# Kernel tuning notes

Measured on AMD Instinct MI355X. Metric: run time of the kernel, lower is better.

The kernel has to match this reference:

```python
import jax, jax.numpy as jnp
import numpy as np

N_NODES = 100000
N_EDGES = 1_000_000
NODE_DIM = 64
EDGE_DIM = 32
HIDDEN = 64


def _unif(key, shape, fan_in):
    bound = 1.0 / np.sqrt(fan_in)
    return jax.random.uniform(key, shape, jnp.float32, -bound, bound)


def setup_inputs() -> dict:
    key = jax.random.key(0)
    ks = jax.random.split(key, 11)
    node_features = jax.random.normal(ks[0], (N_NODES, NODE_DIM), jnp.float32)
    edge_index = jax.random.randint(ks[1], (2, N_EDGES), 0, N_NODES, dtype=jnp.int64)
    edge_features = jax.random.normal(ks[2], (N_EDGES, EDGE_DIM), jnp.float32)
    in_dim = 2 * NODE_DIM + EDGE_DIM
    # message MLP: Linear(in_dim, HIDDEN) -> ReLU -> Linear(HIDDEN, HIDDEN)
    W1 = _unif(ks[3], (HIDDEN, in_dim), in_dim)
    b1 = _unif(ks[4], (HIDDEN,), in_dim)
    W2 = _unif(ks[5], (HIDDEN, HIDDEN), HIDDEN)
    b2 = _unif(ks[6], (HIDDEN,), HIDDEN)
    # GRUCell(input=HIDDEN, hidden=NODE_DIM); gates stacked [r; z; n]
    w_ih = _unif(ks[7], (3 * NODE_DIM, HIDDEN), NODE_DIM)
    w_hh = _unif(ks[8], (3 * NODE_DIM, NODE_DIM), NODE_DIM)
    b_ih = _unif(ks[9], (3 * NODE_DIM,), NODE_DIM)
    b_hh = _unif(ks[10], (3 * NODE_DIM,), NODE_DIM)
    return {
        "node_features": node_features,
        "edge_index": edge_index,
        "edge_features": edge_features,
        "W1": W1, "b1": b1, "W2": W2, "b2": b2,
        "w_ih": w_ih, "w_hh": w_hh, "b_ih": b_ih, "b_hh": b_hh,
    }


def reference(node_features, edge_index, edge_features, W1, b1, W2, b2, w_ih, w_hh, b_ih, b_hh):
    src, dst = edge_index[0], edge_index[1]
    # gather endpoints and build message MLP input: [E, 2*node_dim+edge_dim]
    x = jnp.concatenate([node_features[src], node_features[dst], edge_features], axis=-1)
    h = jax.nn.relu(x @ W1.T + b1)
    messages = h @ W2.T + b2  # [E, HIDDEN]
    # scatter-add into per-node aggregates
    agg = jax.ops.segment_sum(messages, dst, num_segments=node_features.shape[0])
    # GRUCell(agg, node_features) with torch gate order [r, z, n]
    gi = agg @ w_ih.T + b_ih
    gh = node_features @ w_hh.T + b_hh
    i_r, i_z, i_n = jnp.split(gi, 3, axis=-1)
    h_r, h_z, h_n = jnp.split(gh, 3, axis=-1)
    r = jax.nn.sigmoid(i_r + h_r)
    z = jax.nn.sigmoid(i_z + h_z)
    n = jnp.tanh(i_n + r * h_n)
    return (1.0 - z) * n + z * node_features
```

## Files before the change

kernel.cpp:

```cpp
#include <hip/hip_runtime.h>
#include <hip/hip_bf16.h>

#define N_NODES 100000
#define N_EDGES 1000000

typedef __bf16 bf16x8 __attribute__((ext_vector_type(8)));
typedef float  f32x4  __attribute__((ext_vector_type(4)));

#define MFMA(a, b, c) __builtin_amdgcn_mfma_f32_16x16x32_bf16((a), (b), (c), 0, 0, 0)

__device__ __forceinline__ float sigmoid_f(float x) { return 1.f / (1.f + __expf(-x)); }
__device__ __forceinline__ float tanh_f(float x) {
    float cx = fminf(fmaxf(x, -30.f), 30.f);
    float e = __expf(-2.f * cx);
    return (1.f - e) / (1.f + e);
}

__global__ __launch_bounds__(256) void pq_kernel(
    const float* __restrict__ nf, const float* __restrict__ W1,
    const float* __restrict__ b1,
    __bf16* __restrict__ Pb, __bf16* __restrict__ Qb)
{
    const int lane = threadIdx.x & 63;
    const int r = lane & 15, g = lane >> 4;

    bf16x8 Bs[4][2], Bd[4][2];
    #pragma unroll
    for (int nt = 0; nt < 4; ++nt)
        #pragma unroll
        for (int kk = 0; kk < 2; ++kk) {
            const float* ws = &W1[(nt * 16 + r) * 160 + kk * 32 + g * 8];
            const float* wd = ws + 64;
            f32x4 s0 = *(const f32x4*)ws, s1 = *(const f32x4*)(ws + 4);
            f32x4 d0 = *(const f32x4*)wd, d1 = *(const f32x4*)(wd + 4);
            #pragma unroll
            for (int j = 0; j < 4; ++j) {
                Bs[nt][kk][j] = (__bf16)s0[j]; Bs[nt][kk][j + 4] = (__bf16)s1[j];
                Bd[nt][kk][j] = (__bf16)d0[j]; Bd[nt][kk][j + 4] = (__bf16)d1[j];
            }
        }
    float b1v[4];
    #pragma unroll
    for (int nt = 0; nt < 4; ++nt) b1v[nt] = b1[nt * 16 + r];

    const int wid = blockIdx.x * (blockDim.x >> 6) + (threadIdx.x >> 6);
    const int nW  = gridDim.x * (blockDim.x >> 6);
    for (int t = wid; t < N_NODES / 16; t += nW) {
        const int base = t * 16;
        bf16x8 A[2];
        #pragma unroll
        for (int kk = 0; kk < 2; ++kk) {
            const float* p = &nf[(size_t)(base + r) * 64 + kk * 32 + g * 8];
            f32x4 v0 = *(const f32x4*)p, v1 = *(const f32x4*)(p + 4);
            #pragma unroll
            for (int j = 0; j < 4; ++j) { A[kk][j] = (__bf16)v0[j]; A[kk][j + 4] = (__bf16)v1[j]; }
        }
        f32x4 accP[4] = {}, accQ[4] = {};
        #pragma unroll
        for (int nt = 0; nt < 4; ++nt)
            #pragma unroll
            for (int kk = 0; kk < 2; ++kk) {
                accP[nt] = MFMA(A[kk], Bs[nt][kk], accP[nt]);
                accQ[nt] = MFMA(A[kk], Bd[nt][kk], accQ[nt]);
            }
        #pragma unroll
        for (int nt = 0; nt < 4; ++nt)
            #pragma unroll
            for (int rr = 0; rr < 4; ++rr) {
                const int node = base + g * 4 + rr;
                const int col  = nt * 16 + r;
                Pb[(size_t)node * 64 + col] = (__bf16)(accP[nt][rr] + b1v[nt]);
                Qb[(size_t)node * 64 + col] = (__bf16)accQ[nt][rr];
            }
    }
}

#define LDH 68
__global__ __launch_bounds__(256) void edge_kernel(
    const int* __restrict__ ei, const float* __restrict__ ef,
    const float* __restrict__ W1, const float* __restrict__ W2,
    const float* __restrict__ b2,
    const __bf16* __restrict__ Pb, const __bf16* __restrict__ Qb,
    float* __restrict__ agg)
{
    __shared__ float lds_h[4][16 * LDH];
    const int lane = threadIdx.x & 63;
    const int r = lane & 15, g = lane >> 4;
    float* hb = lds_h[threadIdx.x >> 6];
    const int* srcI = ei;
    const int* dstI = ei + N_EDGES;

    bf16x8 Be[4];
    #pragma unroll
    for (int nt = 0; nt < 4; ++nt) {
        const float* w = &W1[(nt * 16 + r) * 160 + 128 + g * 8];
        f32x4 w0 = *(const f32x4*)w, w1 = *(const f32x4*)(w + 4);
        #pragma unroll
        for (int j = 0; j < 4; ++j) { Be[nt][j] = (__bf16)w0[j]; Be[nt][j + 4] = (__bf16)w1[j]; }
    }
    bf16x8 B2[4][2];
    #pragma unroll
    for (int nt = 0; nt < 4; ++nt)
        #pragma unroll
        for (int kk = 0; kk < 2; ++kk) {
            const float* w = &W2[(nt * 16 + r) * 64 + kk * 32 + g * 8];
            f32x4 w0 = *(const f32x4*)w, w1 = *(const f32x4*)(w + 4);
            #pragma unroll
            for (int j = 0; j < 4; ++j) { B2[nt][kk][j] = (__bf16)w0[j]; B2[nt][kk][j + 4] = (__bf16)w1[j]; }
        }
    float b2v[4];
    #pragma unroll
    for (int nt = 0; nt < 4; ++nt) b2v[nt] = b2[nt * 16 + r];

    const int wid = blockIdx.x * (blockDim.x >> 6) + (threadIdx.x >> 6);
    const int nW  = gridDim.x * (blockDim.x >> 6);
    for (int t = wid; t < N_EDGES / 16; t += nW) {
        const int base = t * 16;
        const int er = base + r;
        const int es = srcI[er], ed = dstI[er];

        bf16x8 Ae;
        {
            const float* p = &ef[(size_t)er * 32 + g * 8];
            f32x4 v0 = *(const f32x4*)p, v1 = *(const f32x4*)(p + 4);
            #pragma unroll
            for (int j = 0; j < 4; ++j) { Ae[j] = (__bf16)v0[j]; Ae[j + 4] = (__bf16)v1[j]; }
        }
        f32x4 accT[4] = {};
        #pragma unroll
        for (int nt = 0; nt < 4; ++nt) accT[nt] = MFMA(Ae, Be[nt], accT[nt]);

        #pragma unroll
        for (int nt = 0; nt < 4; ++nt)
            #pragma unroll
            for (int rr = 0; rr < 4; ++rr)
                hb[(g * 4 + rr) * LDH + nt * 16 + r] = accT[nt][rr];

        bf16x8 A2[2];
        #pragma unroll
        for (int kk = 0; kk < 2; ++kk) {
            const int k = kk * 32 + g * 8;
            const float* hp = &hb[r * LDH + k];
            f32x4 h0 = *(const f32x4*)hp, h1 = *(const f32x4*)(hp + 4);
            bf16x8 p8 = *(const bf16x8*)(Pb + (size_t)es * 64 + k);
            bf16x8 q8 = *(const bf16x8*)(Qb + (size_t)ed * 64 + k);
            #pragma unroll
            for (int j = 0; j < 4; ++j) {
                A2[kk][j]     = (__bf16)fmaxf(h0[j] + (float)p8[j]     + (float)q8[j],     0.f);
                A2[kk][j + 4] = (__bf16)fmaxf(h1[j] + (float)p8[j + 4] + (float)q8[j + 4], 0.f);
            }
        }
        f32x4 accM[4] = {};
        #pragma unroll
        for (int nt = 0; nt < 4; ++nt)
            #pragma unroll
            for (int kk = 0; kk < 2; ++kk)
                accM[nt] = MFMA(A2[kk], B2[nt][kk], accM[nt]);

        int4 d4 = *(const int4*)(dstI + base + g * 4);
        const int* dd = (const int*)&d4;
        #pragma unroll
        for (int rr = 0; rr < 4; ++rr) {
            float* dp = agg + (size_t)dd[rr] * 64;
            #pragma unroll
            for (int nt = 0; nt < 4; ++nt)
                atomicAdd(dp + nt * 16 + r, accM[nt][rr] + b2v[nt]);
        }
    }
}

__global__ __launch_bounds__(256) void gru_kernel(
    const float* __restrict__ nf, const float* __restrict__ agg,
    const float* __restrict__ w_ih, const float* __restrict__ w_hh,
    const float* __restrict__ b_ih, const float* __restrict__ b_hh,
    float* __restrict__ out)
{
    const int lane = threadIdx.x & 63;
    const int r = lane & 15, g = lane >> 4;
    const int wid = blockIdx.x * (blockDim.x >> 6) + (threadIdx.x >> 6);
    const int nW  = gridDim.x * (blockDim.x >> 6);

    float br[4], bz[4], bin_[4], bhn_[4];
    #pragma unroll
    for (int nt = 0; nt < 4; ++nt) {
        const int d = nt * 16 + r;
        br[nt]   = b_ih[d] + b_hh[d];
        bz[nt]   = b_ih[64 + d] + b_hh[64 + d];
        bin_[nt] = b_ih[128 + d];
        bhn_[nt] = b_hh[128 + d];
    }

    for (int t = wid; t < N_NODES / 16; t += nW) {
        const int base = t * 16;
        bf16x8 aaH[2], aaL[2], ahH[2], ahL[2];
        #pragma unroll
        for (int kk = 0; kk < 2; ++kk) {
            const float* pa = &agg[(size_t)(base + r) * 64 + kk * 32 + g * 8];
            const float* ph = &nf [(size_t)(base + r) * 64 + kk * 32 + g * 8];
            f32x4 a0 = *(const f32x4*)pa, a1 = *(const f32x4*)(pa + 4);
            f32x4 h0 = *(const f32x4*)ph, h1 = *(const f32x4*)(ph + 4);
            #pragma unroll
            for (int j = 0; j < 4; ++j) {
                float av0 = a0[j], av1 = a1[j], hv0 = h0[j], hv1 = h1[j];
                __bf16 x;
                x = (__bf16)av0; aaH[kk][j]     = x; aaL[kk][j]     = (__bf16)(av0 - (float)x);
                x = (__bf16)av1; aaH[kk][j + 4] = x; aaL[kk][j + 4] = (__bf16)(av1 - (float)x);
                x = (__bf16)hv0; ahH[kk][j]     = x; ahL[kk][j]     = (__bf16)(hv0 - (float)x);
                x = (__bf16)hv1; ahH[kk][j + 4] = x; ahL[kk][j + 4] = (__bf16)(hv1 - (float)x);
            }
        }

        f32x4 accR[4] = {}, accZ[4] = {}, accIN[4] = {}, accHN[4] = {};
        #pragma unroll
        for (int c = 0; c < 3; ++c) {
            bf16x8 Bi[4][2], Bh[4][2];
            #pragma unroll
            for (int nt = 0; nt < 4; ++nt)
                #pragma unroll
                for (int kk = 0; kk < 2; ++kk) {
                    const float* wi = &w_ih[(size_t)(c * 64 + nt * 16 + r) * 64 + kk * 32 + g * 8];
                    const float* wh = &w_hh[(size_t)(c * 64 + nt * 16 + r) * 64 + kk * 32 + g * 8];
                    f32x4 i0 = *(const f32x4*)wi, i1 = *(const f32x4*)(wi + 4);
                    f32x4 h0 = *(const f32x4*)wh, h1 = *(const f32x4*)(wh + 4);
                    #pragma unroll
                    for (int j = 0; j < 4; ++j) {
                        Bi[nt][kk][j] = (__bf16)i0[j]; Bi[nt][kk][j + 4] = (__bf16)i1[j];
                        Bh[nt][kk][j] = (__bf16)h0[j]; Bh[nt][kk][j + 4] = (__bf16)h1[j];
                    }
                }
            #pragma unroll
            for (int nt = 0; nt < 4; ++nt) {
                f32x4 ai = {}, ah = {};
                #pragma unroll
                for (int kk = 0; kk < 2; ++kk) {
                    ai = MFMA(aaH[kk], Bi[nt][kk], ai);
                    ai = MFMA(aaL[kk], Bi[nt][kk], ai);
                    ah = MFMA(ahH[kk], Bh[nt][kk], ah);
                    ah = MFMA(ahL[kk], Bh[nt][kk], ah);
                }
                if (c == 0)      accR[nt] = ai + ah;
                else if (c == 1) accZ[nt] = ai + ah;
                else             { accIN[nt] = ai; accHN[nt] = ah; }
            }
        }
        #pragma unroll
        for (int nt = 0; nt < 4; ++nt)
            #pragma unroll
            for (int rr = 0; rr < 4; ++rr) {
                const int node = base + g * 4 + rr;
                const int d    = nt * 16 + r;
                float rg = sigmoid_f(accR[nt][rr] + br[nt]);
                float zg = sigmoid_f(accZ[nt][rr] + bz[nt]);
                float ng = tanh_f(accIN[nt][rr] + bin_[nt] + rg * (accHN[nt][rr] + bhn_[nt]));
                float hv = nf[(size_t)node * 64 + d];
                out[(size_t)node * 64 + d] = (1.f - zg) * ng + zg * hv;
            }
    }
}

extern "C" void kernel_launch(void* const* d_in, const int* in_sizes, int n_in,
                              void* d_out, int out_size, void* d_ws, size_t ws_size,
                              hipStream_t stream) {
    const float* nf  = (const float*)d_in[0];
    const int*   ei  = (const int*)  d_in[1];
    const float* ef  = (const float*)d_in[2];
    const float* W1  = (const float*)d_in[3];
    const float* b1  = (const float*)d_in[4];
    const float* W2  = (const float*)d_in[5];
    const float* b2  = (const float*)d_in[6];
    const float* wih = (const float*)d_in[7];
    const float* whh = (const float*)d_in[8];
    const float* bih = (const float*)d_in[9];
    const float* bhh = (const float*)d_in[10];
    float* out = (float*)d_out;

    char* ws = (char*)d_ws;
    const size_t aggBytes = (size_t)N_NODES * 64 * 4;
    const size_t pqBytes  = (size_t)N_NODES * 64 * 2;
    float*  agg = (float*)ws;
    __bf16* Pb  = (__bf16*)(ws + aggBytes);
    __bf16* Qb  = (__bf16*)(ws + aggBytes + pqBytes);

    hipMemsetAsync(agg, 0, aggBytes, stream);
    pq_kernel<<<1563, 256, 0, stream>>>(nf, W1, b1, Pb, Qb);
    edge_kernel<<<2048, 256, 0, stream>>>(ei, ef, W1, W2, b2, Pb, Qb, agg);
    gru_kernel<<<1563, 256, 0, stream>>>(nf, agg, wih, whh, bih, bhh, out);
}
```

Measured before the change: 536.1 us.

## Fold second message linear into GRU via degree-weighted aggregation and atomic-free gather

Because W2 is linear, the sum of messages equals W2 applied to the sum of ReLU hidden activations plus degree times b2. The new path precomputes M = w_ih·W2 and b2 projected through w_ih, aggregates only the ReLU hidden vectors per destination node, and adds a degree-scaled bias in the GRU. Edges are bucketed by destination with a counting scatter into fixed-capacity slots so each node's sum is gathered by one wavefront without float atomics, with an overflow path that still uses atomics. The cost is a materialized 128MB bf16 edge projection buffer, a large slot array and extra kernel launches. A fallback to the old fused edge kernel runs when the workspace is too small.

```diff
diff --git a/kernel.cpp b/kernel.cpp
--- a/kernel.cpp
+++ b/kernel.cpp
@@ -3,6 +3,8 @@
 
 #define N_NODES 100000
 #define N_EDGES 1000000
+#define CAP 64
+#define OVF_CAP 65536
 
 typedef __bf16 bf16x8 __attribute__((ext_vector_type(8)));
 typedef float  f32x4  __attribute__((ext_vector_type(4)));
@@ -75,20 +77,12 @@
     }
 }
 
-#define LDH 68
-__global__ __launch_bounds__(256) void edge_kernel(
-    const int* __restrict__ ei, const float* __restrict__ ef,
-    const float* __restrict__ W1, const float* __restrict__ W2,
-    const float* __restrict__ b2,
-    const __bf16* __restrict__ Pb, const __bf16* __restrict__ Qb,
-    float* __restrict__ agg)
-{
-    __shared__ float lds_h[4][16 * LDH];
+__global__ __launch_bounds__(256) void e_kernel(
+    const float* __restrict__ ef, const float* __restrict__ W1,
+    __bf16* __restrict__ Eb)
+{
     const int lane = threadIdx.x & 63;
     const int r = lane & 15, g = lane >> 4;
-    float* hb = lds_h[threadIdx.x >> 6];
-    const int* srcI = ei;
-    const int* dstI = ei + N_EDGES;
 
     bf16x8 Be[4];
     #pragma unroll
@@ -98,30 +92,14 @@
         #pragma unroll
         for (int j = 0; j < 4; ++j) { Be[nt][j] = (__bf16)w0[j]; Be[nt][j + 4] = (__bf16)w1[j]; }
     }
-    bf16x8 B2[4][2];
-    #pragma unroll
-    for (int nt = 0; nt < 4; ++nt)
-        #pragma unroll
-        for (int kk = 0; kk < 2; ++kk) {
-            const float* w = &W2[(nt * 16 + r) * 64 + kk * 32 + g * 8];
-            f32x4 w0 = *(const f32x4*)w, w1 = *(const f32x4*)(w + 4);
-            #pragma unroll
-            for (int j = 0; j < 4; ++j) { B2[nt][kk][j] = (__bf16)w0[j]; B2[nt][kk][j + 4] = (__bf16)w1[j]; }
-        }
-    float b2v[4];
-    #pragma unroll
-    for (int nt = 0; nt < 4; ++nt) b2v[nt] = b2[nt * 16 + r];
 
     const int wid = blockIdx.x * (blockDim.x >> 6) + (threadIdx.x >> 6);
     const int nW  = gridDim.x * (blockDim.x >> 6);
     for (int t = wid; t < N_EDGES / 16; t += nW) {
         const int base = t * 16;
-        const int er = base + r;
-        const int es = srcI[er], ed = dstI[er];
-
         bf16x8 Ae;
         {
-            const float* p = &ef[(size_t)er * 32 + g * 8];
+            const float* p = &ef[(size_t)(base + r) * 32 + g * 8];
             f32x4 v0 = *(const f32x4*)p, v1 = *(const f32x4*)(p + 4);
             #pragma unroll
             for (int j = 0; j < 4; ++j) { Ae[j] = (__bf16)v0[j]; Ae[j + 4] = (__bf16)v1[j]; }
@@ -129,50 +107,107 @@
         f32x4 accT[4] = {};
         #pragma unroll
         for (int nt = 0; nt < 4; ++nt) accT[nt] = MFMA(Ae, Be[nt], accT[nt]);
-
         #pragma unroll
         for (int nt = 0; nt < 4; ++nt)
             #pragma unroll
             for (int rr = 0; rr < 4; ++rr)
-                hb[(g * 4 + rr) * LDH + nt * 16 + r] = accT[nt][rr];
-
-        bf16x8 A2[2];
-        #pragma unroll
-        for (int kk = 0; kk < 2; ++kk) {
-            const int k = kk * 32 + g * 8;
-            const float* hp = &hb[r * LDH + k];
-            f32x4 h0 = *(const f32x4*)hp, h1 = *(const f32x4*)(hp + 4);
-            bf16x8 p8 = *(const bf16x8*)(Pb + (size_t)es * 64 + k);
-            bf16x8 q8 = *(const bf16x8*)(Qb + (size_t)ed * 64 + k);
-            #pragma unroll
-            for (int j = 0; j < 4; ++j) {
-                A2[kk][j]     = (__bf16)fmaxf(h0[j] + (float)p8[j]     + (float)q8[j],     0.f);
-                A2[kk][j + 4] = (__bf16)fmaxf(h1[j] + (float)p8[j + 4] + (float)q8[j + 4], 0.f);
-            }
-        }
-        f32x4 accM[4] = {};
-        #pragma unroll
-        for (int nt = 0; nt < 4; ++nt)
-            #pragma unroll
-            for (int kk = 0; kk < 2; ++kk)
-                accM[nt] = MFMA(A2[kk], B2[nt][kk], accM[nt]);
-
-        int4 d4 = *(const int4*)(dstI + base + g * 4);
-        const int* dd = (const int*)&d4;
-        #pragma unroll
-        for (int rr = 0; rr < 4; ++rr) {
-            float* dp = agg + (size_t)dd[rr] * 64;
-            #pragma unroll
-            for (int nt = 0; nt < 4; ++nt)
-                atomicAdd(dp + nt * 16 + r, accM[nt][rr] + b2v[nt]);
-        }
+                Eb[(size_t)(base + g * 4 + rr) * 64 + nt * 16 + r] = (__bf16)accT[nt][rr];
+    }
+}
+
+__global__ __launch_bounds__(256) void scatter_kernel(
+    const int* __restrict__ ei, int* __restrict__ cnt,
+    int2* __restrict__ slots, int* __restrict__ ovf)
+{
+    const int* srcI = ei;
+    const int* dstI = ei + N_EDGES;
+    int* ovfCnt = cnt + N_NODES;
+    for (int e = blockIdx.x * blockDim.x + threadIdx.x; e < N_EDGES;
+         e += gridDim.x * blockDim.x) {
+        int d = dstI[e];
+        int r = atomicAdd(&cnt[d], 1);
+        if (r < CAP) slots[(size_t)d * CAP + r] = make_int2(e, srcI[e]);
+        else { int o = atomicAdd(ovfCnt, 1); if (o < OVF_CAP) ovf[o] = e; }
+    }
+}
+
+__global__ __launch_bounds__(256) void gather_kernel(
+    const int* __restrict__ cnt, const int2* __restrict__ slots,
+    const __bf16* __restrict__ Eb, const __bf16* __restrict__ Pb,
+    const __bf16* __restrict__ Qb, float* __restrict__ Hsum)
+{
+    const int lane = threadIdx.x & 63;
+    const int wid = blockIdx.x * (blockDim.x >> 6) + (threadIdx.x >> 6);
+    const int nW  = gridDim.x * (blockDim.x >> 6);
+    for (int n = wid; n < N_NODES; n += nW) {
+        const int c = cnt[n];
+        const int m = min(c, CAP);
+        int2 sl = slots[(size_t)n * CAP + lane];
+        float q = (float)Qb[(size_t)n * 64 + lane];
+        float acc = 0.f;
+        float ev = 0.f, pv = 0.f;
+        if (m > 0) {
+            int e0 = __shfl(sl.x, 0), s0 = __shfl(sl.y, 0);
+            ev = (float)Eb[(size_t)e0 * 64 + lane];
+            pv = (float)Pb[(size_t)s0 * 64 + lane];
+        }
+        for (int it = 0; it < m; ++it) {
+            float ce = ev, cp = pv;
+            if (it + 1 < m) {
+                int e1 = __shfl(sl.x, it + 1), s1 = __shfl(sl.y, it + 1);
+                ev = (float)Eb[(size_t)e1 * 64 + lane];
+                pv = (float)Pb[(size_t)s1 * 64 + lane];
+            }
+            acc += fmaxf(ce + cp + q, 0.f);
+        }
+        Hsum[(size_t)n * 64 + lane] = acc;
+    }
+}
+
+__global__ void ovf_kernel(
+    const int* __restrict__ cnt, const int* __restrict__ ovf,
+    const int* __restrict__ ei,
+    const __bf16* __restrict__ Eb, const __bf16* __restrict__ Pb,
+    const __bf16* __restrict__ Qb, float* __restrict__ Hsum)
+{
+    const int lane = threadIdx.x;
+    int nv = min(cnt[N_NODES], OVF_CAP);
+    const int* srcI = ei;
+    const int* dstI = ei + N_EDGES;
+    for (int i = blockIdx.x; i < nv; i += gridDim.x) {
+        int e = ovf[i];
+        int d = dstI[e], s = srcI[e];
+        float v = fmaxf((float)Eb[(size_t)e * 64 + lane] +
+                        (float)Pb[(size_t)s * 64 + lane] +
+                        (float)Qb[(size_t)d * 64 + lane], 0.f);
+        atomicAdd(&Hsum[(size_t)d * 64 + lane], v);
+    }
+}
+
+__global__ __launch_bounds__(256) void prep_kernel(
+    const float* __restrict__ w_ih, const float* __restrict__ W2,
+    const float* __restrict__ b2, float* __restrict__ M, float* __restrict__ b2i)
+{
+    int tid = blockIdx.x * blockDim.x + threadIdx.x;
+    if (tid < 192 * 64) {
+        int d = tid >> 6, k = tid & 63;
+        float s = 0.f;
+        #pragma unroll 8
+        for (int j = 0; j < 64; ++j) s += w_ih[d * 64 + j] * W2[j * 64 + k];
+        M[tid] = s;
+    }
+    if (tid < 192) {
+        float s = 0.f;
+        for (int j = 0; j < 64; ++j) s += w_ih[tid * 64 + j] * b2[j];
+        b2i[tid] = s;
     }
 }
 
 __global__ __launch_bounds__(256) void gru_kernel(
-    const float* __restrict__ nf, const float* __restrict__ agg,
-    const float* __restrict__ w_ih, const float* __restrict__ w_hh,
+    const float* __restrict__ nf, const float* __restrict__ Hsum,
+    const float* __restrict__ M, const float* __restrict__ w_hh,
     const float* __restrict__ b_ih, const float* __restrict__ b_hh,
+    const float* __restrict__ b2i, const int* __restrict__ cnt,
     float* __restrict__ out)
 {
     const int lane = threadIdx.x & 63;
@@ -181,6 +216,7 @@
     const int nW  = gridDim.x * (blockDim.x >> 6);
 
     float br[4], bz[4], bin_[4], bhn_[4];
+    float c2r[4], c2z[4], c2n[4];
     #pragma unroll
     for (int nt = 0; nt < 4; ++nt) {
         const int d = nt * 16 + r;
@@ -188,6 +224,9 @@
         bz[nt]   = b_ih[64 + d] + b_hh[64 + d];
         bin_[nt] = b_ih[128 + d];
         bhn_[nt] = b_hh[128 + d];
+        c2r[nt] = b2i ? b2i[d] : 0.f;
+        c2z[nt] = b2i ? b2i[64 + d] : 0.f;
+        c2n[nt] = b2i ? b2i[128 + d] : 0.f;
     }
 
     for (int t = wid; t < N_NODES / 16; t += nW) {
@@ -195,8 +234,8 @@
         bf16x8 aaH[2], aaL[2], ahH[2], ahL[2];
         #pragma unroll
         for (int kk = 0; kk < 2; ++kk) {
-            const float* pa = &agg[(size_t)(base + r) * 64 + kk * 32 + g * 8];
-            const float* ph = &nf [(size_t)(base + r) * 64 + kk * 32 + g * 8];
+            const float* pa = &Hsum[(size_t)(base + r) * 64 + kk * 32 + g * 8];
+            const float* ph = &nf  [(size_t)(base + r) * 64 + kk * 32 + g * 8];
             f32x4 a0 = *(const f32x4*)pa, a1 = *(const f32x4*)(pa + 4);
             f32x4 h0 = *(const f32x4*)ph, h1 = *(const f32x4*)(ph + 4);
             #pragma unroll
@@ -218,7 +257,7 @@
             for (int nt = 0; nt < 4; ++nt)
                 #pragma unroll
                 for (int kk = 0; kk < 2; ++kk) {
-                    const float* wi = &w_ih[(size_t)(c * 64 + nt * 16 + r) * 64 + kk * 32 + g * 8];
+                    const float* wi = &M   [(size_t)(c * 64 + nt * 16 + r) * 64 + kk * 32 + g * 8];
                     const float* wh = &w_hh[(size_t)(c * 64 + nt * 16 + r) * 64 + kk * 32 + g * 8];
                     f32x4 i0 = *(const f32x4*)wi, i1 = *(const f32x4*)(wi + 4);
                     f32x4 h0 = *(const f32x4*)wh, h1 = *(const f32x4*)(wh + 4);
@@ -249,12 +288,104 @@
             for (int rr = 0; rr < 4; ++rr) {
                 const int node = base + g * 4 + rr;
                 const int d    = nt * 16 + r;
-                float rg = sigmoid_f(accR[nt][rr] + br[nt]);
-                float zg = sigmoid_f(accZ[nt][rr] + bz[nt]);
-                float ng = tanh_f(accIN[nt][rr] + bin_[nt] + rg * (accHN[nt][rr] + bhn_[nt]));
+                float dg = cnt ? (float)cnt[node] : 0.f;
+                float rg = sigmoid_f(accR[nt][rr] + br[nt] + dg * c2r[nt]);
+                float zg = sigmoid_f(accZ[nt][rr] + bz[nt] + dg * c2z[nt]);
+                float ng = tanh_f(accIN[nt][rr] + bin_[nt] + dg * c2n[nt] +
+                                  rg * (accHN[nt][rr] + bhn_[nt]));
                 float hv = nf[(size_t)node * 64 + d];
                 out[(size_t)node * 64 + d] = (1.f - zg) * ng + zg * hv;
             }
+    }
+}
+
+#define LDH 68
+__global__ __launch_bounds__(256) void edge_kernel_fb(
+    const int* __restrict__ ei, const float* __restrict__ ef,
+    const float* __restrict__ W1, const float* __restrict__ W2,
+    const float* __restrict__ b2,
+    const __bf16* __restrict__ Pb, const __bf16* __restrict__ Qb,
+    float* __restrict__ agg)
+{
+    __shared__ float lds_h[4][16 * LDH];
+    const int lane = threadIdx.x & 63;
+    const int r = lane & 15, g = lane >> 4;
+    float* hb = lds_h[threadIdx.x >> 6];
+    const int* srcI = ei;
+    const int* dstI = ei + N_EDGES;
+
+    bf16x8 Be[4];
+    #pragma unroll
+    for (int nt = 0; nt < 4; ++nt) {
+        const float* w = &W1[(nt * 16 + r) * 160 + 128 + g * 8];
+        f32x4 w0 = *(const f32x4*)w, w1 = *(const f32x4*)(w + 4);
+        #pragma unroll
+        for (int j = 0; j < 4; ++j) { Be[nt][j] = (__bf16)w0[j]; Be[nt][j + 4] = (__bf16)w1[j]; }
+    }
+    bf16x8 B2[4][2];
+    #pragma unroll
+    for (int nt = 0; nt < 4; ++nt)
+        #pragma unroll
+        for (int kk = 0; kk < 2; ++kk) {
+            const float* w = &W2[(nt * 16 + r) * 64 + kk * 32 + g * 8];
+            f32x4 w0 = *(const f32x4*)w, w1 = *(const f32x4*)(w + 4);
+            #pragma unroll
+            for (int j = 0; j < 4; ++j) { B2[nt][kk][j] = (__bf16)w0[j]; B2[nt][kk][j + 4] = (__bf16)w1[j]; }
+        }
+    float b2v[4];
+    #pragma unroll
+    for (int nt = 0; nt < 4; ++nt) b2v[nt] = b2[nt * 16 + r];
+
+    const int wid = blockIdx.x * (blockDim.x >> 6) + (threadIdx.x >> 6);
+    const int nW  = gridDim.x * (blockDim.x >> 6);
+    for (int t = wid; t < N_EDGES / 16; t += nW) {
+        const int base = t * 16;
+        const int er = base + r;
+        const int es = srcI[er], ed = dstI[er];
+        bf16x8 Ae;
+        {
+            const float* p = &ef[(size_t)er * 32 + g * 8];
+            f32x4 v0 = *(const f32x4*)p, v1 = *(const f32x4*)(p + 4);
+            #pragma unroll
+            for (int j = 0; j < 4; ++j) { Ae[j] = (__bf16)v0[j]; Ae[j + 4] = (__bf16)v1[j]; }
+        }
+        f32x4 accT[4] = {};
+        #pragma unroll
+        for (int nt = 0; nt < 4; ++nt) accT[nt] = MFMA(Ae, Be[nt], accT[nt]);
+        #pragma unroll
+        for (int nt = 0; nt < 4; ++nt)
+            #pragma unroll
+            for (int rr = 0; rr < 4; ++rr)
+                hb[(g * 4 + rr) * LDH + nt * 16 + r] = accT[nt][rr];
+        bf16x8 A2[2];
+        #pragma unroll
+        for (int kk = 0; kk < 2; ++kk) {
+            const int k = kk * 32 + g * 8;
+            const float* hp = &hb[r * LDH + k];
+            f32x4 h0 = *(const f32x4*)hp, h1 = *(const f32x4*)(hp + 4);
+            bf16x8 p8 = *(const bf16x8*)(Pb + (size_t)es * 64 + k);
+            bf16x8 q8 = *(const bf16x8*)(Qb + (size_t)ed * 64 + k);
+            #pragma unroll
+            for (int j = 0; j < 4; ++j) {
+                A2[kk][j]     = (__bf16)fmaxf(h0[j] + (float)p8[j]     + (float)q8[j],     0.f);
+                A2[kk][j + 4] = (__bf16)fmaxf(h1[j] + (float)p8[j + 4] + (float)q8[j + 4], 0.f);
+            }
+        }
+        f32x4 accM[4] = {};
+        #pragma unroll
+        for (int nt = 0; nt < 4; ++nt)
+            #pragma unroll
+            for (int kk = 0; kk < 2; ++kk)
+                accM[nt] = MFMA(A2[kk], B2[nt][kk], accM[nt]);
+        int4 d4 = *(const int4*)(dstI + base + g * 4);
+        const int* dd = (const int*)&d4;
+        #pragma unroll
+        for (int rr = 0; rr < 4; ++rr) {
+            float* dp = agg + (size_t)dd[rr] * 64;
+            #pragma unroll
+            for (int nt = 0; nt < 4; ++nt)
+                atomicAdd(dp + nt * 16 + r, accM[nt][rr] + b2v[nt]);
+        }
     }
 }
 
@@ -275,14 +406,35 @@
     float* out = (float*)d_out;
 
     char* ws = (char*)d_ws;
-    const size_t aggBytes = (size_t)N_NODES * 64 * 4;
-    const size_t pqBytes  = (size_t)N_NODES * 64 * 2;
-    float*  agg = (float*)ws;
-    __bf16* Pb  = (__bf16*)(ws + aggBytes);
-    __bf16* Qb  = (__bf16*)(ws + aggBytes + pqBytes);
-
-    hipMemsetAsync(agg, 0, aggBytes, stream);
-    pq_kernel<<<1563, 256, 0, stream>>>(nf, W1, b1, Pb, Qb);
-    edge_kernel<<<2048, 256, 0, stream>>>(ei, ef, W1, W2, b2, Pb, Qb, agg);
-    gru_kernel<<<1563, 256, 0, stream>>>(nf, agg, wih, whh, bih, bhh, out);
-}
+    size_t off = 0;
+    auto alloc = [&](size_t bytes) { char* p = ws + off; off = (off + bytes + 255) & ~(size_t)255; return p; };
+    int*    cnt   = (int*)   alloc((size_t)(N_NODES + 1) * 4);
+    int*    ovf   = (int*)   alloc((size_t)OVF_CAP * 4);
+    int2*   slots = (int2*)  alloc((size_t)N_NODES * CAP * 8);
+    __bf16* Eb    = (__bf16*)alloc((size_t)N_EDGES * 64 * 2);
+    __bf16* Pb    = (__bf16*)alloc((size_t)N_NODES * 64 * 2);
+    __bf16* Qb    = (__bf16*)alloc((size_t)N_NODES * 64 * 2);
+    float*  Hsum  = (float*) alloc((size_t)N_NODES * 64 * 4);
+    float*  M     = (float*) alloc((size_t)192 * 64 * 4);
+    float*  b2i   = (float*) alloc((size_t)192 * 4);
+    const size_t need = off;
+
+    if (ws_size >= need) {
+        hipMemsetAsync(cnt, 0, (size_t)(N_NODES + 1) * 4, stream);
+        pq_kernel     <<<1563, 256, 0, stream>>>(nf, W1, b1, Pb, Qb);
+        e_kernel      <<<2048, 256, 0, stream>>>(ef, W1, Eb);
+        scatter_kernel<<<2048, 256, 0, stream>>>(ei, cnt, slots, ovf);
+        prep_kernel   <<<48,   256, 0, stream>>>(wih, W2, b2, M, b2i);
+        gather_kernel <<<25000, 256, 0, stream>>>(cnt, slots, Eb, Pb, Qb, Hsum);
+        ovf_kernel    <<<16,   64,  0, stream>>>(cnt, ovf, ei, Eb, Pb, Qb, Hsum);
+        gru_kernel    <<<1563, 256, 0, stream>>>(nf, Hsum, M, whh, bih, bhh, b2i, cnt, out);
+    } else {
+        float*  agg = (float*)ws;
+        __bf16* Pf  = (__bf16*)(ws + (size_t)N_NODES * 64 * 4);
+        __bf16* Qf  = (__bf16*)(ws + (size_t)N_NODES * 64 * 4 + (size_t)N_NODES * 64 * 2);
+        hipMemsetAsync(agg, 0, (size_t)N_NODES * 64 * 4, stream);
+        pq_kernel     <<<1563, 256, 0, stream>>>(nf, W1, b1, Pf, Qf);
+        edge_kernel_fb<<<2048, 256, 0, stream>>>(ei, ef, W1, W2, b2, Pf, Qf, agg);
+        gru_kernel    <<<1563, 256, 0, stream>>>(nf, agg, wih, whh, bih, bhh, nullptr, nullptr, out);
+    }
+}
```

New measurement: 616.2 us. +14.9%, slower.
